# Kernel optimization log

Hardware: AMD Instinct MI355X
Metric: run time of the kernel (lower is better)

Reference implementation:

```python
import jax, jax.numpy as jnp
import numpy as np

B, L = 4, 2048
D_MODEL, D_INNER, D_STATE, DT_RANK, K = 512, 1024, 16, 64, 4


def setup_inputs() -> dict:
    key = jax.random.key(0)
    ks = jax.random.split(key, 21)
    def n(k, shape, s=0.02):
        return (jax.random.normal(k, shape) * s).astype(jnp.float32)
    inp = {"x": jax.random.normal(ks[0], (B, L, D_MODEL), jnp.float32)}
    for i, sfx in enumerate(("f", "b")):
        o = 1 + i * 8
        inp[f"W_in_{sfx}"] = n(ks[o], (2 * D_INNER, D_MODEL))
        inp[f"conv_w_{sfx}"] = n(ks[o + 1], (D_INNER, 1, K), 0.1)
        inp[f"conv_b_{sfx}"] = jnp.zeros((D_INNER,), jnp.float32)
        inp[f"A_log_{sfx}"] = (jax.random.normal(ks[o + 2], (D_STATE, D_INNER)) * 0.1).astype(jnp.float32)
        inp[f"D_{sfx}"] = jnp.ones((D_INNER,), jnp.float32)
        inp[f"Wx_{sfx}"] = n(ks[o + 3], (DT_RANK + 2 * D_STATE, D_INNER))
        inp[f"Wdt_{sfx}"] = n(ks[o + 4], (D_INNER, DT_RANK), DT_RANK ** -0.5)
        dt = jnp.exp(jax.random.uniform(ks[o + 5], (D_INNER,)) * (np.log(0.1) - np.log(0.001)) + np.log(0.001))
        inp[f"bdt_{sfx}"] = (dt + jnp.log(-jnp.expm1(-dt))).astype(jnp.float32)
        inp[f"Wout_{sfx}"] = n(ks[o + 6], (D_MODEL, D_INNER))
    return inp


def _mamba_block(x, W_in, conv_w, conv_b, A_log, Dp, Wx, Wdt, bdt, Wout):
    # x: [B, L, d_model]
    xz = jnp.einsum('bld,ed->ble', x, W_in)              # [B, L, 2*d_inner]
    xb, zb = xz[..., :D_INNER], xz[..., D_INNER:]
    # causal depthwise conv over time
    xc = jnp.transpose(xb, (0, 2, 1))                     # [B, M, L]
    xc = jax.lax.conv_general_dilated(
        xc, conv_w, window_strides=(1,), padding=[(K - 1, 0)],
        feature_group_count=D_INNER,
        dimension_numbers=('NCH', 'OIH', 'NCH')) + conv_b[None, :, None]
    xb = jax.nn.silu(jnp.transpose(xc, (0, 2, 1)))        # [B, L, M]
    # input-dependent SSM parameters
    proj = jnp.einsum('blm,pm->blp', xb, Wx)              # [B, L, dt_rank+2D]
    dt_in = proj[..., :DT_RANK]
    Bs = proj[..., DT_RANK:DT_RANK + D_STATE]             # [B, L, D]
    Cs = proj[..., DT_RANK + D_STATE:]                    # [B, L, D]
    dt = jax.nn.softplus(jnp.einsum('blr,mr->blm', dt_in, Wdt) + bdt)  # [B, L, M]
    A_T = -jnp.exp(A_log).T                               # [M, D]

    def step(h, inp):
        dt_t, x_t, B_t, C_t = inp                         # [B,M],[B,M],[B,D],[B,D]
        dA = jnp.exp(dt_t[:, :, None] * A_T[None])        # [B, M, D]
        h = dA * h + (dt_t * x_t)[:, :, None] * B_t[:, None, :]
        y_t = jnp.einsum('bmd,bd->bm', h, C_t)
        return h, y_t

    xs = (jnp.moveaxis(dt, 1, 0), jnp.moveaxis(xb, 1, 0),
          jnp.moveaxis(Bs, 1, 0), jnp.moveaxis(Cs, 1, 0))
    h0 = jnp.zeros((x.shape[0], D_INNER, D_STATE), x.dtype)
    _, ys = jax.lax.scan(step, h0, xs)                    # [L, B, M]
    y = jnp.moveaxis(ys, 0, 1) + Dp * xb                  # [B, L, M]
    y = y * jax.nn.silu(zb)                               # SiLU gate
    return jnp.einsum('blm,dm->bld', y, Wout)             # [B, L, d_model]


def reference(x,
              W_in_f, conv_w_f, conv_b_f, A_log_f, D_f, Wx_f, Wdt_f, bdt_f, Wout_f,
              W_in_b, conv_w_b, conv_b_b, A_log_b, D_b, Wx_b, Wdt_b, bdt_b, Wout_b):
    out_f = _mamba_block(x, W_in_f, conv_w_f, conv_b_f, A_log_f, D_f, Wx_f, Wdt_f, bdt_f, Wout_f)
    out_b = jnp.flip(_mamba_block(jnp.flip(x, 1), W_in_b, conv_w_b, conv_b_b, A_log_b, D_b, Wx_b, Wdt_b, bdt_b, Wout_b), 1)
    return out_f + out_b
```

## Files before the change

### kernel.cpp

```cpp
#include <hip/hip_runtime.h>
#include <hip/hip_bf16.h>
#include <cstdint>
#include <cstdio>

typedef float f32x4 __attribute__((ext_vector_type(4)));
typedef float f32x2 __attribute__((ext_vector_type(2)));
typedef short s16x8 __attribute__((ext_vector_type(8)));
typedef unsigned int u32x2 __attribute__((ext_vector_type(2)));

__device__ __forceinline__ float us2f(unsigned short u){
  union { unsigned int i; float f; } v; v.i = ((unsigned int)u) << 16; return v.f;
}
__device__ __forceinline__ unsigned short f2us(float f){
  union { float f; unsigned int i; } v; v.f = f;
  unsigned int r = v.i + 0x7fffu + ((v.i >> 16) & 1u);
  return (unsigned short)(r >> 16);
}
__device__ __forceinline__ void gload_lds16(const void* g, void* l){
  __builtin_amdgcn_global_load_lds(
      (const __attribute__((address_space(1))) unsigned int*)g,
      (__attribute__((address_space(3))) unsigned int*)l, 16, 0, 0);
}

#define PK0 0.999962f

__global__ __launch_bounds__(256)
void prep_k(const float* __restrict__ x,
            const float* __restrict__ W_in_f, const float* __restrict__ W_in_b,
            const float* __restrict__ Wx_f,   const float* __restrict__ Wx_b,
            const float* __restrict__ Wdt_f,  const float* __restrict__ Wdt_b,
            const float* __restrict__ Wout_f, const float* __restrict__ Wout_b,
            const float* __restrict__ Alog_f, const float* __restrict__ Alog_b,
            const float* __restrict__ bdt_f,  const float* __restrict__ bdt_b,
            unsigned short* __restrict__ W1cat, unsigned short* __restrict__ Wxpad,
            unsigned short* __restrict__ Wdtb,  unsigned short* __restrict__ Woutcat,
            float* __restrict__ A2, float* __restrict__ bdtcat,
            unsigned short* __restrict__ xbf, float* __restrict__ Cf)
{
  long i = (long)blockIdx.x * 256 + threadIdx.x;
  if (i < 4194304) {
    xbf[i] = f2us(x[i]); return;
  }
  i -= 4194304;
  if (i < 2097152) {
    int n = (int)(i >> 9), k = (int)(i & 511);
    float v = (n < 2048) ? W_in_f[(long)n*512 + k] : W_in_b[(long)(n-2048)*512 + k];
    W1cat[i] = f2us(v); return;
  }
  i -= 2097152;
  if (i < 262144) {
    int dir = (int)(i >> 17); long r = i & 131071; int n = (int)(r >> 10), k = (int)(r & 1023);
    const float* Wx = dir ? Wx_b : Wx_f;
    Wxpad[(long)dir*131072 + r] = f2us(n < 96 ? Wx[(long)n*1024 + k] : 0.f); return;
  }
  i -= 262144;
  if (i < 131072) {
    int dir = (int)(i >> 16); long r = i & 65535;
    Wdtb[i] = f2us((dir ? Wdt_b : Wdt_f)[r]); return;
  }
  i -= 131072;
  if (i < 1048576) {
    int n = (int)(i >> 11), k = (int)(i & 2047);
    float v = (k < 1024) ? Wout_f[(long)n*1024 + k] : Wout_b[(long)n*1024 + (k-1024)];
    Woutcat[i] = f2us(v); return;
  }
  i -= 1048576;
  if (i < 32768) {
    int dir = (int)(i >> 14); long r = i & 16383; int m = (int)(r >> 4), d = (int)(r & 15);
    const float* Al = dir ? Alog_b : Alog_f;
    A2[i] = -__expf(Al[(long)d*1024 + m]) * 1.4426950408889634f; return;
  }
  i -= 32768;
  if (i < 2048) {
    int dir = (int)(i >> 10), m = (int)(i & 1023);
    bdtcat[i] = (dir ? bdt_b : bdt_f)[m]; return;
  }
  i -= 2048;
  if (i < 98304) {
    int dir = (int)(i / 49152); long r = i % 49152;
    int m = (int)(r / 48), j = (int)(r % 48);
    int k = j >> 4, d = j & 15;
    const float* Al = dir ? Alog_b : Alog_f;
    const float w = -__expf(Al[(long)d*1024 + m]);
    float c;
    if (k == 0)      c = 0.999150f * w;
    else if (k == 1) c = 0.492809f * w * w;
    else             c = 0.139212f * w * w * w;
    Cf[(long)dir*49152 + (long)m*48 + (k << 4) + d] = c;
    return;
  }
}

template<int OUT_MODE>
__global__ __launch_bounds__(256)
void gemm_bt(const unsigned short* __restrict__ Ap, const unsigned short* __restrict__ Bp,
             void* __restrict__ Cp, const float* __restrict__ biasp,
             float* __restrict__ bcf,
             int K, int lda, int ldb, int ldc,
             long az, long bz, long cz, int biasz)
{
  const int z   = blockIdx.z;
  const int tid = threadIdx.x;
  const int bm  = blockIdx.x, bn = blockIdx.y;

  __shared__ __align__(16) unsigned short Ash[128][64];
  __shared__ __align__(16) unsigned short Bsh[128][64];

  const int wave = tid >> 6, lane = tid & 63;
  const int wr = (wave >> 1) << 6, wc = (wave & 1) << 6;
  const int fr = lane & 15, fs = lane >> 4;

  const int rr  = tid >> 3;
  const int csp = tid & 7;
  const int csg = ((csp ^ (rr & 7)) << 3);

  const unsigned short* Ag = Ap + (long)z * az;
  const unsigned short* Bg = Bp + (long)z * bz;

  const long abase = (long)(bm*128 + rr)*lda + csg;
  const long bbase = (long)(bn*128 + rr)*ldb + csg;
  unsigned short* lA = &Ash[rr][csp << 3];
  unsigned short* lB = &Bsh[rr][csp << 3];

  f32x4 acc[4][4];
  #pragma unroll
  for (int i=0;i<4;i++)
    #pragma unroll
    for (int j=0;j<4;j++) acc[i][j] = (f32x4){0.f,0.f,0.f,0.f};

  const int NK = K >> 6;
  for (int ks = 0; ks < NK; ++ks){
    const long k0 = (long)ks << 6;
    __syncthreads();
    #pragma unroll
    for (int r=0;r<4;r++){
      gload_lds16(Ag + abase + (long)(r*32)*lda + k0, lA + r*32*64);
      gload_lds16(Bg + bbase + (long)(r*32)*ldb + k0, lB + r*32*64);
    }
    __syncthreads();

    #pragma unroll
    for (int sub=0; sub<2; ++sub){
      s16x8 af[4], bfv[4];
      #pragma unroll
      for (int i=0;i<4;i++){
        const int ar = wr + i*16 + fr;
        af[i]  = *(const s16x8*)&Ash[ar][(((sub<<2)+fs) ^ (fr&7)) << 3];
        const int br = wc + i*16 + fr;
        bfv[i] = *(const s16x8*)&Bsh[br][(((sub<<2)+fs) ^ (fr&7)) << 3];
      }
      #pragma unroll
      for (int i=0;i<4;i++)
        #pragma unroll
        for (int j=0;j<4;j++)
          acc[i][j] = __builtin_amdgcn_mfma_f32_16x16x32_bf16(bfv[j], af[i], acc[i][j], 0, 0, 0);
    }
  }

  #pragma unroll
  for (int i=0;i<4;i++){
    const int row = bm*128 + wr + i*16 + fr;
    #pragma unroll
    for (int j=0;j<4;j++){
      const int c0 = bn*128 + wc + j*16 + (fs << 2);
      f32x4 v = acc[i][j];
      const long cbase = (long)z*cz + (long)row*ldc + c0;
      if (OUT_MODE == 2){
        *(f32x4*)((float*)Cp + cbase) = v;
      } else if (OUT_MODE == 1){
        const f32x4 b4 = *(const f32x4*)(biasp + z*biasz + c0);
        u32x2 o;
        unsigned short s[4];
        #pragma unroll
        for (int e=0;e<4;e++){
          float t = v[e] + b4[e];
          t = fmaxf(t, 0.f) + log1pf(__expf(-fabsf(t)));
          s[e] = f2us(t);
        }
        o[0] = (unsigned int)s[0] | ((unsigned int)s[1] << 16);
        o[1] = (unsigned int)s[2] | ((unsigned int)s[3] << 16);
        *(u32x2*)((unsigned short*)Cp + cbase) = o;
      } else {
        u32x2 o;
        o[0] = (unsigned int)f2us(v[0]) | ((unsigned int)f2us(v[1]) << 16);
        o[1] = (unsigned int)f2us(v[2]) | ((unsigned int)f2us(v[3]) << 16);
        *(u32x2*)((unsigned short*)Cp + cbase) = o;
        if (OUT_MODE == 3 && c0 >= 64 && c0 < 96){
          *(f32x4*)(bcf + ((long)z*8192 + row)*32 + (c0 - 64)) = v;
        }
      }
    }
  }
}

__global__ __launch_bounds__(256)
void conv_silu_k(const unsigned short* __restrict__ xz,
                 const float* __restrict__ wf, const float* __restrict__ cbf,
                 const float* __restrict__ wb, const float* __restrict__ cbb,
                 unsigned short* __restrict__ xbc)
{
  const int tid = threadIdx.x;
  const long tok = blockIdx.x;
  const int l   = (int)(tok & 2047);
  const int dir = tid >> 7;
  const int mg  = (tid & 127) << 3;
  const float* w  = dir ? wb  : wf;
  const float* cb = dir ? cbb : cbf;
  const long rowb = tok << 12;
  const int  xcol = (dir << 11) + mg;

  f32x4 wv[8];
  #pragma unroll
  for (int e=0;e<8;e++) wv[e] = *(const f32x4*)(w + (mg + e)*4);
  const f32x4 cb0 = *(const f32x4*)(cb + mg);
  const f32x4 cb1 = *(const f32x4*)(cb + mg + 4);

  float acc[8];
  #pragma unroll
  for (int e=0;e<4;e++){ acc[e]=cb0[e]; acc[4+e]=cb1[e]; }

  #pragma unroll
  for (int k=0;k<4;k++){
    const int off = dir ? (3 - k) : (k - 3);
    const int pos = l + off;
    if (pos >= 0 && pos < 2048){
      const s16x8 xv = *(const s16x8*)(xz + rowb + ((long)off << 12) + xcol);
      #pragma unroll
      for (int e=0;e<8;e++)
        acc[e] = __builtin_fmaf(wv[e][k], us2f((unsigned short)xv[e]), acc[e]);
    }
  }
  s16x8 out;
  #pragma unroll
  for (int e=0;e<8;e++){
    const float s = acc[e] / (1.f + __expf(-acc[e]));
    out[e] = (short)f2us(s);
  }
  *(s16x8*)(xbc + tok*2048 + (dir << 10) + mg) = out;
}

#define SCHUNK 32
#define NCHUNK 64

__global__ __launch_bounds__(256)
void scan1_k(const unsigned short* __restrict__ dtb, const unsigned short* __restrict__ xbc,
             const float* __restrict__ BCf, const float* __restrict__ Cf,
             unsigned short* __restrict__ hloc, float* __restrict__ Ssum)
{
  const int tidx = threadIdx.x;
  const int cb = blockIdx.x, c = blockIdx.y, bz = blockIdx.z;
  const int b = bz >> 1, dir = bz & 1;
  const int m = cb*256 + tidx;

  float C1[16], C2[16], C3[16];
  { const f32x4* p = (const f32x4*)(Cf + ((long)dir*1024 + m)*48);
    #pragma unroll
    for (int q=0;q<4;q++){
      f32x4 v1=p[q], v2=p[q+4], v3=p[q+8];
      #pragma unroll
      for (int e=0;e<4;e++){ C1[q*4+e]=v1[e]; C2[q*4+e]=v2[e]; C3[q*4+e]=v3[e]; } } }

  const int  l0 = dir ? (2047 - c*SCHUNK) : (c*SCHUNK);
  const int  ls = dir ? -1 : 1;
  const long tok0 = (long)b*2048 + l0;
  const unsigned short* dtp = dtb + (((long)dir) << 23) + tok0*1024 + m;
  const unsigned short* xvp = xbc + tok0*2048 + (dir << 10) + m;
  const float* bcp = BCf + ((long)dir*8192 + tok0)*32;
  const long dstp = (long)ls*1024, xstp = (long)ls*2048, bstp = (long)ls*32;

  float h[16];
  #pragma unroll
  for (int d=0;d<16;d++) h[d]=0.f;
  float S = 0.f;

  unsigned short du = *dtp, xu = *xvp;
  for (int t=0;t<SCHUNK;t++){
    const float dt = us2f(du), xv = us2f(xu);
    dtp += dstp; xvp += xstp;
    du = *dtp; xu = *xvp;
    S += dt;
    const float u = dt * xv;
    const float dt2 = dt*dt, dt3 = dt2*dt;
    const f32x4 bv0 = *(const f32x4*)(bcp);
    const f32x4 bv1 = *(const f32x4*)(bcp + 4);
    const f32x4 bv2 = *(const f32x4*)(bcp + 8);
    const f32x4 bv3 = *(const f32x4*)(bcp + 12);
    bcp += bstp;
    #pragma unroll
    for (int d=0;d<16;d++){
      const float bval = (d<4)? bv0[d&3] : (d<8)? bv1[d&3] : (d<12)? bv2[d&3] : bv3[d&3];
      float a = __builtin_fmaf(C1[d], dt, PK0);
      a = __builtin_fmaf(C2[d], dt2, a);
      a = __builtin_fmaf(C3[d], dt3, a);
      h[d] = __builtin_fmaf(a, h[d], u * bval);
    }
  }
  const long o = (((long)bz * NCHUNK) + c)*1024 + m;
  s16x8 hv0, hv1;
  #pragma unroll
  for (int e=0;e<8;e++){ hv0[e] = (short)f2us(h[e]); hv1[e] = (short)f2us(h[8+e]); }
  *(s16x8*)(hloc + (o << 4))     = hv0;
  *(s16x8*)(hloc + (o << 4) + 8) = hv1;
  Ssum[o] = S;
}

__global__ __launch_bounds__(256)
void scan2_k(const float* __restrict__ A2, const float* __restrict__ Ssum,
             unsigned short* __restrict__ hloc)
{
  const long idx = (long)blockIdx.x*256 + threadIdx.x;
  const long bz = idx >> 14; const int r = (int)(idx & 16383);
  const int dir = (int)(bz & 1);
  const float a2 = A2[((long)dir << 14) + r];
  const long base = bz * NCHUNK;
  float hs = 0.f;
  float hlN = us2f(hloc[base*16384 + r]);
  float SN  = Ssum[base*1024 + (r >> 4)];
  for (int c=0;c<NCHUNK;c++){
    const float hl = hlN, Sv = SN;
    const int cn = (c+1 < NCHUNK) ? c+1 : c;
    hlN = us2f(hloc[(base+cn)*16384 + r]);
    SN  = Ssum[(base+cn)*1024 + (r >> 4)];
    const float P = __builtin_amdgcn_exp2f(a2 * Sv);
    hloc[(base+c)*16384 + r] = f2us(hs);
    hs = __builtin_fmaf(P, hs, hl);
  }
}

__global__ __launch_bounds__(256)
void scan3_k(const unsigned short* __restrict__ dtb, const unsigned short* __restrict__ xbc,
             const float* __restrict__ BCf, const float* __restrict__ Cf,
             const unsigned short* __restrict__ hstart, const unsigned short* __restrict__ xz,
             const float* __restrict__ D_f, const float* __restrict__ D_b,
             unsigned short* __restrict__ ybuf)
{
  const int tidx = threadIdx.x;
  const int cb = blockIdx.x, c = blockIdx.y, bz = blockIdx.z;
  const int b = bz >> 1, dir = bz & 1;
  const int m = cb*256 + tidx;

  float C1[16], C2[16], C3[16];
  { const f32x4* p = (const f32x4*)(Cf + ((long)dir*1024 + m)*48);
    #pragma unroll
    for (int q=0;q<4;q++){
      f32x4 v1=p[q], v2=p[q+4], v3=p[q+8];
      #pragma unroll
      for (int e=0;e<4;e++){ C1[q*4+e]=v1[e]; C2[q*4+e]=v2[e]; C3[q*4+e]=v3[e]; } } }
  const float Dm = (dir ? D_b : D_f)[m];

  float h[16];
  { const long o = ((((long)bz*NCHUNK) + c)*1024 + m) << 4;
    s16x8 hv0 = *(const s16x8*)(hstart + o);
    s16x8 hv1 = *(const s16x8*)(hstart + o + 8);
    #pragma unroll
    for (int e=0;e<8;e++){ h[e] = us2f((unsigned short)hv0[e]);
                           h[8+e] = us2f((unsigned short)hv1[e]); } }

  const int  l0 = dir ? (2047 - c*SCHUNK) : (c*SCHUNK);
  const int  ls = dir ? -1 : 1;
  const long tok0 = (long)b*2048 + l0;
  const unsigned short* dtp = dtb + (((long)dir) << 23) + tok0*1024 + m;
  const unsigned short* xvp = xbc + tok0*2048 + (dir << 10) + m;
  const unsigned short* zp  = xz  + (tok0 << 12) + (dir << 11) + 1024 + m;
  unsigned short*       yp  = ybuf + tok0*2048 + (dir << 10) + m;
  const float* bcp = BCf + ((long)dir*8192 + tok0)*32;
  const long dstp = (long)ls*1024, xstp = (long)ls*2048, zstp = (long)ls << 12;
  const long bstp = (long)ls*32;

  unsigned short du = *dtp, xu = *xvp, zu = *zp;
  for (int t=0;t<SCHUNK;t++){
    const float dt = us2f(du), xv = us2f(xu), zb = us2f(zu);
    dtp += dstp; xvp += xstp; zp += zstp;
    du = *dtp; xu = *xvp; zu = *zp;
    const float u = dt * xv;
    const float dt2 = dt*dt, dt3 = dt2*dt;
    const f32x4 bv0 = *(const f32x4*)(bcp);
    const f32x4 bv1 = *(const f32x4*)(bcp + 4);
    const f32x4 bv2 = *(const f32x4*)(bcp + 8);
    const f32x4 bv3 = *(const f32x4*)(bcp + 12);
    const f32x4 cv0 = *(const f32x4*)(bcp + 16);
    const f32x4 cv1 = *(const f32x4*)(bcp + 20);
    const f32x4 cv2 = *(const f32x4*)(bcp + 24);
    const f32x4 cv3 = *(const f32x4*)(bcp + 28);
    bcp += bstp;
    float y0=0.f, y1=0.f;
    #pragma unroll
    for (int d=0;d<16;d++){
      const float bval = (d<4)? bv0[d&3] : (d<8)? bv1[d&3] : (d<12)? bv2[d&3] : bv3[d&3];
      const float cval = (d<4)? cv0[d&3] : (d<8)? cv1[d&3] : (d<12)? cv2[d&3] : cv3[d&3];
      float a = __builtin_fmaf(C1[d], dt, PK0);
      a = __builtin_fmaf(C2[d], dt2, a);
      a = __builtin_fmaf(C3[d], dt3, a);
      h[d] = __builtin_fmaf(a, h[d], u * bval);
      if (d & 1) y1 = __builtin_fmaf(h[d], cval, y1);
      else       y0 = __builtin_fmaf(h[d], cval, y0);
    }
    const float y = (y0 + y1) + Dm * xv;
    const float gate = zb / (1.f + __expf(-zb));
    *yp = f2us(y * gate);
    yp += xstp;
  }
}

extern "C" void kernel_launch(void* const* d_in, const int* in_sizes, int n_in,
                              void* d_out, int out_size, void* d_ws, size_t ws_size,
                              hipStream_t stream)
{
  const float* x      = (const float*)d_in[0];
  const float* W_in_f = (const float*)d_in[1];
  const float* convw_f= (const float*)d_in[2];
  const float* convb_f= (const float*)d_in[3];
  const float* Alog_f = (const float*)d_in[4];
  const float* D_f    = (const float*)d_in[5];
  const float* Wx_f   = (const float*)d_in[6];
  const float* Wdt_f  = (const float*)d_in[7];
  const float* bdt_f  = (const float*)d_in[8];
  const float* Wout_f = (const float*)d_in[9];
  const float* W_in_b = (const float*)d_in[10];
  const float* convw_b= (const float*)d_in[11];
  const float* convb_b= (const float*)d_in[12];
  const float* Alog_b = (const float*)d_in[13];
  const float* D_b    = (const float*)d_in[14];
  const float* Wx_b   = (const float*)d_in[15];
  const float* Wdt_b  = (const float*)d_in[16];
  const float* bdt_b  = (const float*)d_in[17];
  const float* Wout_b = (const float*)d_in[18];

  char* w = (char*)d_ws;
  auto carve = [&](size_t bytes) -> char* {
    char* p = w; w += (bytes + 255) & ~(size_t)255; return p;
  };
  unsigned short* W1cat   = (unsigned short*)carve(4096ULL*512*2);
  unsigned short* Wxpad   = (unsigned short*)carve(2ULL*128*1024*2);
  unsigned short* Wdtb    = (unsigned short*)carve(2ULL*1024*64*2);
  unsigned short* Woutcat = (unsigned short*)carve(512ULL*2048*2);
  float*          A2      = (float*)carve(2ULL*1024*16*4);
  float*          bdtcat  = (float*)carve(2048ULL*4);
  float*          Cf      = (float*)carve(2ULL*1024*48*4);
  float*          BCf     = (float*)carve(2ULL*8192*32*4);
  unsigned short* xz      = (unsigned short*)carve(8192ULL*4096*2);
  unsigned short* xbc     = (unsigned short*)carve(8192ULL*2048*2);
  unsigned short* proj    = (unsigned short*)carve(2ULL*8192*128*2);
  unsigned short* dtb     = (unsigned short*)carve(2ULL*8192*1024*2);
  unsigned short* ybuf    = (unsigned short*)carve(8192ULL*2048*2);
  unsigned short* hloc    = (unsigned short*)carve(8ULL*NCHUNK*1024*16*2);
  float*          Ssum    = (float*)carve(8ULL*NCHUNK*1024*4);
  unsigned short* xbf     = ybuf;

  if ((size_t)(w - (char*)d_ws) > ws_size) {
    fprintf(stderr, "kernel_launch: ws too small (%zu needed, %zu given)\n",
            (size_t)(w - (char*)d_ws), ws_size);
    return;
  }

  prep_k<<<dim3(30728), 256, 0, stream>>>(x, W_in_f, W_in_b, Wx_f, Wx_b, Wdt_f, Wdt_b,
                                          Wout_f, Wout_b, Alog_f, Alog_b, bdt_f, bdt_b,
                                          W1cat, Wxpad, Wdtb, Woutcat, A2, bdtcat, xbf, Cf);
  gemm_bt<0><<<dim3(64,32,1), 256, 0, stream>>>(xbf, W1cat, xz, nullptr, nullptr,
                                                512, 512, 512, 4096, 0, 0, 0, 0);
  conv_silu_k<<<dim3(8192), 256, 0, stream>>>(xz, convw_f, convb_f, convw_b, convb_b, xbc);
  gemm_bt<3><<<dim3(64,1,2), 256, 0, stream>>>(xbc, Wxpad, proj, nullptr, BCf,
                                               1024, 2048, 1024, 128,
                                               1024, 131072, 1048576, 0);
  gemm_bt<1><<<dim3(64,8,2), 256, 0, stream>>>(proj, Wdtb, dtb, bdtcat, nullptr,
                                               64, 128, 64, 1024,
                                               1048576, 65536, 8388608, 1024);
  scan1_k<<<dim3(4,NCHUNK,8), 256, 0, stream>>>(dtb, xbc, BCf, Cf, hloc, Ssum);
  scan2_k<<<dim3(512), 256, 0, stream>>>(A2, Ssum, hloc);
  scan3_k<<<dim3(4,NCHUNK,8), 256, 0, stream>>>(dtb, xbc, BCf, Cf, hloc, xz, D_f, D_b, ybuf);
  gemm_bt<2><<<dim3(64,4,1), 256, 0, stream>>>(ybuf, Woutcat, d_out, nullptr, nullptr,
                                               2048, 2048, 2048, 512, 0, 0, 0, 0);
}
```

Baseline: 322.7 us.

## Stage per-chunk B/C in LDS, use 32-bit offsets, and fuse SiLU gate into input GEMM

```diff
diff --git a/kernel.cpp b/kernel.cpp
--- a/kernel.cpp
+++ b/kernel.cpp
@@ -4,7 +4,6 @@
 #include <cstdio>
 
 typedef float f32x4 __attribute__((ext_vector_type(4)));
-typedef float f32x2 __attribute__((ext_vector_type(2)));
 typedef short s16x8 __attribute__((ext_vector_type(8)));
 typedef unsigned int u32x2 __attribute__((ext_vector_type(2)));
 
@@ -181,6 +180,10 @@
         o[1] = (unsigned int)s[2] | ((unsigned int)s[3] << 16);
         *(u32x2*)((unsigned short*)Cp + cbase) = o;
       } else {
+        if (OUT_MODE == 4 && ((c0 >> 10) & 1)){
+          #pragma unroll
+          for (int e=0;e<4;e++) v[e] = v[e] / (1.f + __expf(-v[e]));
+        }
         u32x2 o;
         o[0] = (unsigned int)f2us(v[0]) | ((unsigned int)f2us(v[1]) << 16);
         o[1] = (unsigned int)f2us(v[2]) | ((unsigned int)f2us(v[3]) << 16);
@@ -262,30 +265,40 @@
 
   const int  l0 = dir ? (2047 - c*SCHUNK) : (c*SCHUNK);
   const int  ls = dir ? -1 : 1;
-  const long tok0 = (long)b*2048 + l0;
-  const unsigned short* dtp = dtb + (((long)dir) << 23) + tok0*1024 + m;
-  const unsigned short* xvp = xbc + tok0*2048 + (dir << 10) + m;
-  const float* bcp = BCf + ((long)dir*8192 + tok0)*32;
-  const long dstp = (long)ls*1024, xstp = (long)ls*2048, bstp = (long)ls*32;
+  const int  tok0 = b*2048 + l0;
+
+  __shared__ float Bs[SCHUNK][16];
+  if (tidx < 128){
+    const int r = tidx >> 2, c4 = (tidx & 3) << 2;
+    *(f32x4*)&Bs[r][c4] =
+        *(const f32x4*)(BCf + ((long)dir*8192 + tok0 + (long)ls*r)*32 + c4);
+  }
+  __syncthreads();
+
+  const unsigned short* dt_base = dtb;
+  const unsigned short* x_base  = xbc - 2048;
+  unsigned odt = (unsigned)((dir << 23) + tok0*1024 + m);
+  unsigned ox  = (unsigned)(2048 + tok0*2048 + (dir << 10) + m);
+  const unsigned sdt = (unsigned)(ls*1024), sx = (unsigned)(ls*2048);
 
   float h[16];
   #pragma unroll
   for (int d=0;d<16;d++) h[d]=0.f;
   float S = 0.f;
 
-  unsigned short du = *dtp, xu = *xvp;
+  unsigned short du = dt_base[odt], xu = x_base[ox];
+  #pragma unroll 2
   for (int t=0;t<SCHUNK;t++){
     const float dt = us2f(du), xv = us2f(xu);
-    dtp += dstp; xvp += xstp;
-    du = *dtp; xu = *xvp;
+    odt += sdt; ox += sx;
+    du = dt_base[odt]; xu = x_base[ox];
     S += dt;
     const float u = dt * xv;
     const float dt2 = dt*dt, dt3 = dt2*dt;
-    const f32x4 bv0 = *(const f32x4*)(bcp);
-    const f32x4 bv1 = *(const f32x4*)(bcp + 4);
-    const f32x4 bv2 = *(const f32x4*)(bcp + 8);
-    const f32x4 bv3 = *(const f32x4*)(bcp + 12);
-    bcp += bstp;
+    const f32x4 bv0 = *(const f32x4*)&Bs[t][0];
+    const f32x4 bv1 = *(const f32x4*)&Bs[t][4];
+    const f32x4 bv2 = *(const f32x4*)&Bs[t][8];
+    const f32x4 bv3 = *(const f32x4*)&Bs[t][12];
     #pragma unroll
     for (int d=0;d<16;d++){
       const float bval = (d<4)? bv0[d&3] : (d<8)? bv1[d&3] : (d<12)? bv2[d&3] : bv3[d&3];
@@ -348,6 +361,15 @@
       for (int e=0;e<4;e++){ C1[q*4+e]=v1[e]; C2[q*4+e]=v2[e]; C3[q*4+e]=v3[e]; } } }
   const float Dm = (dir ? D_b : D_f)[m];
 
+  const int  l0 = dir ? (2047 - c*SCHUNK) : (c*SCHUNK);
+  const int  ls = dir ? -1 : 1;
+  const int  tok0 = b*2048 + l0;
+
+  __shared__ float BC[SCHUNK][32];
+  { const int r = tidx >> 3, c4 = (tidx & 7) << 2;
+    *(f32x4*)&BC[r][c4] =
+        *(const f32x4*)(BCf + ((long)dir*8192 + tok0 + (long)ls*r)*32 + c4); }
+
   float h[16];
   { const long o = ((((long)bz*NCHUNK) + c)*1024 + m) << 4;
     s16x8 hv0 = *(const s16x8*)(hstart + o);
@@ -355,34 +377,33 @@
     #pragma unroll
     for (int e=0;e<8;e++){ h[e] = us2f((unsigned short)hv0[e]);
                            h[8+e] = us2f((unsigned short)hv1[e]); } }
-
-  const int  l0 = dir ? (2047 - c*SCHUNK) : (c*SCHUNK);
-  const int  ls = dir ? -1 : 1;
-  const long tok0 = (long)b*2048 + l0;
-  const unsigned short* dtp = dtb + (((long)dir) << 23) + tok0*1024 + m;
-  const unsigned short* xvp = xbc + tok0*2048 + (dir << 10) + m;
-  const unsigned short* zp  = xz  + (tok0 << 12) + (dir << 11) + 1024 + m;
-  unsigned short*       yp  = ybuf + tok0*2048 + (dir << 10) + m;
-  const float* bcp = BCf + ((long)dir*8192 + tok0)*32;
-  const long dstp = (long)ls*1024, xstp = (long)ls*2048, zstp = (long)ls << 12;
-  const long bstp = (long)ls*32;
-
-  unsigned short du = *dtp, xu = *xvp, zu = *zp;
+  __syncthreads();
+
+  const unsigned short* dt_base = dtb;
+  const unsigned short* x_base  = xbc - 2048;
+  const unsigned short* z_base  = xz  - 4096;
+  unsigned odt = (unsigned)((dir << 23) + tok0*1024 + m);
+  unsigned ox  = (unsigned)(2048 + tok0*2048 + (dir << 10) + m);
+  unsigned oz  = (unsigned)(4096 + tok0*4096 + (dir << 11) + 1024 + m);
+  unsigned oy  = (unsigned)(tok0*2048 + (dir << 10) + m);
+  const unsigned sdt = (unsigned)(ls*1024), sx = (unsigned)(ls*2048), sz = (unsigned)(ls*4096);
+
+  unsigned short du = dt_base[odt], xu = x_base[ox], zu = z_base[oz];
+  #pragma unroll 2
   for (int t=0;t<SCHUNK;t++){
-    const float dt = us2f(du), xv = us2f(xu), zb = us2f(zu);
-    dtp += dstp; xvp += xstp; zp += zstp;
-    du = *dtp; xu = *xvp; zu = *zp;
+    const float dt = us2f(du), xv = us2f(xu), gate = us2f(zu);
+    odt += sdt; ox += sx; oz += sz;
+    du = dt_base[odt]; xu = x_base[ox]; zu = z_base[oz];
     const float u = dt * xv;
     const float dt2 = dt*dt, dt3 = dt2*dt;
-    const f32x4 bv0 = *(const f32x4*)(bcp);
-    const f32x4 bv1 = *(const f32x4*)(bcp + 4);
-    const f32x4 bv2 = *(const f32x4*)(bcp + 8);
-    const f32x4 bv3 = *(const f32x4*)(bcp + 12);
-    const f32x4 cv0 = *(const f32x4*)(bcp + 16);
-    const f32x4 cv1 = *(const f32x4*)(bcp + 20);
-    const f32x4 cv2 = *(const f32x4*)(bcp + 24);
-    const f32x4 cv3 = *(const f32x4*)(bcp + 28);
-    bcp += bstp;
+    const f32x4 bv0 = *(const f32x4*)&BC[t][0];
+    const f32x4 bv1 = *(const f32x4*)&BC[t][4];
+    const f32x4 bv2 = *(const f32x4*)&BC[t][8];
+    const f32x4 bv3 = *(const f32x4*)&BC[t][12];
+    const f32x4 cv0 = *(const f32x4*)&BC[t][16];
+    const f32x4 cv1 = *(const f32x4*)&BC[t][20];
+    const f32x4 cv2 = *(const f32x4*)&BC[t][24];
+    const f32x4 cv3 = *(const f32x4*)&BC[t][28];
     float y0=0.f, y1=0.f;
     #pragma unroll
     for (int d=0;d<16;d++){
@@ -396,9 +417,8 @@
       else       y0 = __builtin_fmaf(h[d], cval, y0);
     }
     const float y = (y0 + y1) + Dm * xv;
-    const float gate = zb / (1.f + __expf(-zb));
-    *yp = f2us(y * gate);
-    yp += xstp;
+    ybuf[oy] = f2us(y * gate);
+    oy += sx;
   }
 }
 
@@ -456,7 +476,7 @@
   prep_k<<<dim3(30728), 256, 0, stream>>>(x, W_in_f, W_in_b, Wx_f, Wx_b, Wdt_f, Wdt_b,
                                           Wout_f, Wout_b, Alog_f, Alog_b, bdt_f, bdt_b,
                                           W1cat, Wxpad, Wdtb, Woutcat, A2, bdtcat, xbf, Cf);
-  gemm_bt<0><<<dim3(64,32,1), 256, 0, stream>>>(xbf, W1cat, xz, nullptr, nullptr,
+  gemm_bt<4><<<dim3(64,32,1), 256, 0, stream>>>(xbf, W1cat, xz, nullptr, nullptr,
                                                 512, 512, 512, 4096, 0, 0, 0, 0);
   conv_silu_k<<<dim3(8192), 256, 0, stream>>>(xz, convw_f, convb_f, convw_b, convb_b, xbc);
   gemm_bt<3><<<dim3(64,1,2), 256, 0, stream>>>(xbc, Wxpad, proj, nullptr, BCf,
```

Measured after the change: 334.2 us. 1.04x slower.
